# Kernel tuning notes

Measured on AMD Instinct MI355X. Metric: run time of the kernel, lower is better.

## Reference

```python
import jax, jax.numpy as jnp
import numpy as np

B, S, HID = 2, 4096, 640
NH, NKV, HD = 4, 1, 256
SCALING = 256.0 ** -0.5
SOFTCAP = 50.0
WINDOW = 512
EPS = 1e-6
ROPE_THETA = 10000.0  # local (sliding) rope base in Gemma3


def _rope_tables(seq_len, dim, theta):
    inv_freq = 1.0 / (theta ** (np.arange(0, dim, 2, dtype=np.float32) / dim))  # [dim/2]
    t = np.arange(seq_len, dtype=np.float32)
    freqs = np.outer(t, inv_freq)                      # [S, dim/2]
    emb = np.concatenate([freqs, freqs], axis=-1)      # [S, dim]
    return np.cos(emb)[None], np.sin(emb)[None]        # [1, S, dim]


def _sliding_causal_mask(b, s, window):
    i = np.arange(s)[:, None]
    j = np.arange(s)[None, :]
    allowed = (j <= i) & (j > i - window)              # causal + sliding window
    mask = np.where(allowed, 0.0, -1e9).astype(np.float32)
    return np.broadcast_to(mask[None, None], (b, 1, s, s)).copy()


def setup_inputs() -> dict:
    key = jax.random.key(0)
    ks = jax.random.split(key, 8)
    cos_np, sin_np = _rope_tables(S, HD, ROPE_THETA)
    return {
        "hidden_states": jax.random.normal(ks[0], (B, S, HID), jnp.float32),
        "cos": jnp.asarray(cos_np),
        "sin": jnp.asarray(sin_np),
        "attention_mask": jnp.asarray(_sliding_causal_mask(B, S, WINDOW)),
        "Wq": jax.random.normal(ks[1], (HID, NH * HD), jnp.float32) * 0.02,
        "Wk": jax.random.normal(ks[2], (HID, NKV * HD), jnp.float32) * 0.02,
        "Wv": jax.random.normal(ks[3], (HID, NKV * HD), jnp.float32) * 0.02,
        "Wo": jax.random.normal(ks[4], (NH * HD, HID), jnp.float32) * 0.02,
        "q_norm_w": jax.random.normal(ks[5], (HD,), jnp.float32) * 0.02,
        "k_norm_w": jax.random.normal(ks[6], (HD,), jnp.float32) * 0.02,
    }


def _rms_norm(x, w):
    var = jnp.mean(jnp.square(x), axis=-1, keepdims=True)
    return x * jax.lax.rsqrt(var + EPS) * (1.0 + w)


def _rotate_half(x):
    x1, x2 = jnp.split(x, 2, axis=-1)
    return jnp.concatenate([-x2, x1], axis=-1)


def _apply_rope(x, cos, sin):
    # x: [B, H, S, D]; cos/sin: [1, S, D] -> unsqueeze head dim
    c = cos[:, None, :, :]
    s = sin[:, None, :, :]
    return x * c + _rotate_half(x) * s


def reference(hidden_states, cos, sin, attention_mask, Wq, Wk, Wv, Wo, q_norm_w, k_norm_w):
    b, s, _ = hidden_states.shape
    # projections (no bias)
    q = (hidden_states @ Wq).reshape(b, s, NH, HD).transpose(0, 2, 1, 3)   # [B,NH,S,D]
    k = (hidden_states @ Wk).reshape(b, s, NKV, HD).transpose(0, 2, 1, 3)  # [B,1,S,D]
    v = (hidden_states @ Wv).reshape(b, s, NKV, HD).transpose(0, 2, 1, 3)  # [B,1,S,D]
    # per-head RMSNorm on q/k
    q = _rms_norm(q, q_norm_w)
    k = _rms_norm(k, k_norm_w)
    # RoPE
    q = _apply_rope(q, cos, sin)
    k = _apply_rope(k, cos, sin)
    # GQA: single kv head broadcast to all query heads
    k2 = k[:, 0]  # [B,S,D]
    v2 = v[:, 0]  # [B,S,D]
    scores = jnp.einsum('bhqd,bkd->bhqk', q, k2) * SCALING
    scores = SOFTCAP * jnp.tanh(scores / SOFTCAP)          # logit softcapping
    scores = scores + attention_mask                        # causal + sliding window
    attn = jax.nn.softmax(scores, axis=-1)
    out = jnp.einsum('bhqk,bkd->bhqd', attn, v2)            # [B,NH,S,D]
    out = out.transpose(0, 2, 1, 3).reshape(b, s, NH * HD)  # [B,S,NH*D]
    return out @ Wo                                         # [B,S,HID]
```

## Files before the change

### kernel.cpp

```cpp
#include <hip/hip_runtime.h>

typedef unsigned short u16;
typedef unsigned int u32;

typedef __attribute__((ext_vector_type(8)))  short bf16x8;
typedef __attribute__((ext_vector_type(4)))  float f32x4;

__device__ __forceinline__ float b2f(u16 u) {
    union { unsigned int i; float f; } v; v.i = ((unsigned int)u) << 16; return v.f;
}
__device__ __forceinline__ u16 f2b(float f) {
    union { float ff; unsigned int i; } v; v.ff = f;
    unsigned int x = v.i;
    return (u16)((x + 0x7fffu + ((x >> 16) & 1u)) >> 16);
}
__device__ __forceinline__ bool detect_bf16(const void* cosT) {
    return ((*(const u32*)cosT) & 0xffffu) == 0x3f80u;
}
__device__ __forceinline__ float4 ld4(const void* p, size_t off, bool isbf) {
    if (isbf) {
        ushort4 v = *(const ushort4*)((const u16*)p + off);
        return make_float4(b2f(v.x), b2f(v.y), b2f(v.z), b2f(v.w));
    }
    return *(const float4*)((const float*)p + off);
}
__device__ __forceinline__ float lds1(const void* p, size_t off, bool isbf) {
    return isbf ? b2f(((const u16*)p)[off]) : ((const float*)p)[off];
}
__device__ __forceinline__ void gll16(const void* g, void* l) {
    __builtin_amdgcn_global_load_lds(
        (const __attribute__((address_space(1))) u32*)g,
        (__attribute__((address_space(3))) u32*)l, 16, 0, 0);
}
__device__ __forceinline__ float capmask(float sdot, int i, int j) {
    float v = sdot * (0.0625f / 50.0f);
    v = fminf(fmaxf(v, -10.0f), 10.0f);
    float e = __expf(2.0f * v);
    float c = 50.0f * (e - 1.0f) / (e + 1.0f);
    bool allowed = (j <= i) && (j > i - 512);
    return allowed ? c : -1e30f;
}

__global__ __launch_bounds__(256) void prep(
    const void* __restrict__ hidden,
    const void* __restrict__ Wq, const void* __restrict__ Wk,
    const void* __restrict__ Wv, const void* __restrict__ Wo,
    const void* __restrict__ cosT,
    u16* __restrict__ Hb, u16* __restrict__ WT, u16* __restrict__ WoT)
{
    const bool isbf = detect_bf16(cosT);
    __shared__ float T[32][33];
    int id = blockIdx.x;
    if (id < 2560) {
        size_t base = ((size_t)id * 256 + threadIdx.x) * 8;
        if (isbf) {
            *(uint4*)(Hb + base) = *(const uint4*)((const u16*)hidden + base);
        } else {
            float4 a = ld4(hidden, base, false);
            float4 b = ld4(hidden, base + 4, false);
            uint4 o;
            o.x = (u32)f2b(a.x) | ((u32)f2b(a.y) << 16);
            o.y = (u32)f2b(a.z) | ((u32)f2b(a.w) << 16);
            o.z = (u32)f2b(b.x) | ((u32)f2b(b.y) << 16);
            o.w = (u32)f2b(b.z) | ((u32)f2b(b.w) << 16);
            *(uint4*)(Hb + base) = o;
        }
        return;
    }
    id -= 2560;
    const int tx = threadIdx.x & 31, ty = threadIdx.x >> 5;
    if (id < 960) {
        const int n0 = (id % 48) * 32, k0 = (id / 48) * 32;
        const void* src; int ldw, nof;
        if (n0 < 1024)      { src = Wq; ldw = 1024; nof = n0; }
        else if (n0 < 1280) { src = Wk; ldw = 256;  nof = n0 - 1024; }
        else                { src = Wv; ldw = 256;  nof = n0 - 1280; }
#pragma unroll
        for (int j = 0; j < 4; j++)
            T[ty + 8 * j][tx] = lds1(src, (size_t)(k0 + ty + 8 * j) * ldw + nof + tx, isbf);
        __syncthreads();
#pragma unroll
        for (int j = 0; j < 4; j++)
            WT[(size_t)(n0 + ty + 8 * j) * 640 + k0 + tx] = f2b(T[tx][ty + 8 * j]);
    } else {
        id -= 960;
        const int k0 = (id & 31) * 32, n0 = (id >> 5) * 32;
#pragma unroll
        for (int j = 0; j < 4; j++)
            T[ty + 8 * j][tx] = lds1(Wo, (size_t)(k0 + ty + 8 * j) * 640 + n0 + tx, isbf);
        __syncthreads();
#pragma unroll
        for (int j = 0; j < 4; j++)
            WoT[(size_t)(n0 + ty + 8 * j) * 1024 + k0 + tx] = f2b(T[tx][ty + 8 * j]);
    }
}

__global__ __launch_bounds__(256) void qkv_gemm(
    const u16* __restrict__ Hb, const u16* __restrict__ WT,
    u16* __restrict__ Qb, u16* __restrict__ Kb, u16* __restrict__ Vtg)
{
    const int n0 = blockIdx.x * 128, m0 = blockIdx.y * 128;
    const int t = threadIdx.x, w = t >> 6, lane = t & 63;
    const int l15 = lane & 15, quad = lane >> 4;
    const int wm = (w & 1) * 64, wn = (w >> 1) * 64;

    __shared__ __align__(16) char smem[33792];

    f32x4 acc[4][4];
#pragma unroll
    for (int i = 0; i < 4; i++)
#pragma unroll
        for (int j = 0; j < 4; j++) acc[i][j] = (f32x4)0.0f;

#pragma unroll
    for (int i = 0; i < 2; i++) {
        int ci = t + 256 * i, m = ci >> 2, c = ci & 3;
        gll16(Hb + (size_t)(m0 + m) * 640 + c * 8, smem + ci * 16);
        gll16(WT + (size_t)(n0 + m) * 640 + c * 8, smem + 8192 + ci * 16);
    }
    __syncthreads();

    for (int it = 0; it < 20; ++it) {
        const int kb = it * 32;
        char* cur = smem + (it & 1) * 16384;
        if (it < 19) {
            char* nxt = smem + ((it + 1) & 1) * 16384;
#pragma unroll
            for (int i = 0; i < 2; i++) {
                int ci = t + 256 * i, m = ci >> 2, c = ci & 3;
                gll16(Hb + (size_t)(m0 + m) * 640 + kb + 32 + c * 8, nxt + ci * 16);
                gll16(WT + (size_t)(n0 + m) * 640 + kb + 32 + c * 8, nxt + 8192 + ci * 16);
            }
        }
        const u16 (*Ah)[32] = (const u16 (*)[32])cur;
        const u16 (*Bh)[32] = (const u16 (*)[32])(cur + 8192);
        bf16x8 af[4], bfr[4];
#pragma unroll
        for (int mi = 0; mi < 4; mi++)
            af[mi] = *(const bf16x8*)&Ah[wm + mi * 16 + l15][quad * 8];
#pragma unroll
        for (int ni = 0; ni < 4; ni++)
            bfr[ni] = *(const bf16x8*)&Bh[wn + ni * 16 + l15][quad * 8];
#pragma unroll
        for (int mi = 0; mi < 4; mi++)
#pragma unroll
            for (int ni = 0; ni < 4; ni++)
                acc[mi][ni] = __builtin_amdgcn_mfma_f32_16x16x32_bf16(
                    af[mi], bfr[ni], acc[mi][ni], 0, 0, 0);
        __syncthreads();
    }

    if (n0 >= 1280) {
        const int bb = m0 >> 12, sblk = m0 & 4095;
#pragma unroll
        for (int mi = 0; mi < 4; mi++)
#pragma unroll
            for (int ni = 0; ni < 4; ni++) {
                int vd = n0 + wn + ni * 16 + l15 - 1280;
                int sb = sblk + wm + mi * 16 + quad * 4;
                ushort4 vv = make_ushort4(f2b(acc[mi][ni][0]), f2b(acc[mi][ni][1]),
                                          f2b(acc[mi][ni][2]), f2b(acc[mi][ni][3]));
                *(ushort4*)(Vtg + (size_t)bb * 1048576 + (size_t)vd * 4096 + sb) = vv;
            }
        return;
    }

    u16 (*Sc)[132] = (u16 (*)[132])smem;
#pragma unroll
    for (int mi = 0; mi < 4; mi++)
#pragma unroll
        for (int ni = 0; ni < 4; ni++)
#pragma unroll
            for (int r = 0; r < 4; r++)
                Sc[wm + mi * 16 + quad * 4 + r][wn + ni * 16 + l15] = f2b(acc[mi][ni][r]);
    __syncthreads();

    u16* dst; int ldo, coff;
    if (n0 < 1024) { dst = Qb; ldo = 1024; coff = n0; }
    else           { dst = Kb; ldo = 256;  coff = n0 - 1024; }
#pragma unroll
    for (int i = 0; i < 8; i++) {
        int idx = t + 256 * i, r = idx >> 4, c = idx & 15;
        *(uint4*)(dst + (size_t)(m0 + r) * ldo + coff + c * 8) = *(const uint4*)&Sc[r][c * 8];
    }
}

__global__ __launch_bounds__(320) void norm_rope(
    u16* __restrict__ Qb, u16* __restrict__ Kb,
    const void* __restrict__ cosT, const void* __restrict__ sinT,
    const void* __restrict__ qw, const void* __restrict__ kw)
{
    const bool isbf = detect_bf16(cosT);
    const int row = blockIdx.x, s = row & 4095;
    const int g = threadIdx.x >> 6, lane = threadIdx.x & 63, d0 = lane * 4;

    u16* p; const void* w;
    if (g < 4) { p = Qb + (size_t)row * 1024 + g * 256 + d0; w = qw; }
    else       { p = Kb + (size_t)row * 256 + d0;            w = kw; }

    ushort4 xv = *(const ushort4*)p;
    float x0 = b2f(xv.x), x1 = b2f(xv.y), x2 = b2f(xv.z), x3 = b2f(xv.w);
    float ssum = x0 * x0 + x1 * x1 + x2 * x2 + x3 * x3;
#pragma unroll
    for (int off = 32; off > 0; off >>= 1) ssum += __shfl_xor(ssum, off, 64);
    float rs = rsqrtf(ssum * (1.0f / 256.0f) + 1e-6f);

    float4 wv = ld4(w, d0, isbf);
    float n0 = x0 * rs * (1.0f + wv.x);
    float n1 = x1 * rs * (1.0f + wv.y);
    float n2 = x2 * rs * (1.0f + wv.z);
    float n3 = x3 * rs * (1.0f + wv.w);

    float o0 = __shfl_xor(n0, 32, 64);
    float o1 = __shfl_xor(n1, 32, 64);
    float o2 = __shfl_xor(n2, 32, 64);
    float o3 = __shfl_xor(n3, 32, 64);
    float sgn = (lane < 32) ? -1.0f : 1.0f;

    float4 cv = ld4(cosT, (size_t)s * 256 + d0, isbf);
    float4 sv = ld4(sinT, (size_t)s * 256 + d0, isbf);
    *(ushort4*)p = make_ushort4(
        f2b(n0 * cv.x + sgn * o0 * sv.x), f2b(n1 * cv.y + sgn * o1 * sv.y),
        f2b(n2 * cv.z + sgn * o2 * sv.z), f2b(n3 * cv.w + sgn * o3 * sv.w));
}

__global__ __launch_bounds__(512, 2) void attn_mfma(
    const u16* __restrict__ Qb, const u16* __restrict__ Kb,
    const u16* __restrict__ Vtg, u16* __restrict__ AO)
{
    const int bx = blockIdx.x;
    const int q0 = (((bx & 7) << 4) + (bx >> 3)) * 32;
    const int b  = blockIdx.y;
    const int t = threadIdx.x, w = t >> 6, lane = t & 63;
    const int h = w & 3, qh = w >> 2;
    const int l15 = lane & 15, quad = lane >> 4;
    const int qbase = q0 + qh * 16;
    const int swz = (l15 & 7) << 4;

    __shared__ __align__(16) u16 Ks[64][256];
    __shared__ __align__(16) u16 Vt[256][64];
    __shared__ __align__(16) u16 Pr[8][16][72];
    __shared__ float l_s[8][16];

    bf16x8 qf[8];
    {
        const u16* qp = Qb + ((size_t)(b * 4096 + qbase + l15)) * 1024 + h * 256 + quad * 8;
#pragma unroll
        for (int s = 0; s < 8; s++) qf[s] = *(const bf16x8*)(qp + s * 32);
    }

    f32x4 o[16];
#pragma unroll
    for (int i = 0; i < 16; i++) o[i] = (f32x4)0.0f;
    float lp[4] = {0.f, 0.f, 0.f, 0.f};

    const int lo = q0 - 511;
    const int jb0 = lo > 0 ? (lo >> 6) << 6 : 0;
    const int jb1 = (q0 + 31) & ~63;

    const u16* kbase = Kb + (size_t)b * 4096 * 256;
    const u16* vbase = Vtg + (size_t)b * 1048576;
    char* const ksb = (char*)&Ks[0][0];
    char* const vtb = (char*)&Vt[0][0];

    for (int jb = jb0; jb <= jb1; jb += 64) {
        __syncthreads();
#pragma unroll
        for (int i = 0; i < 4; i++) {
            int ci = t + 512 * i;
            int kr = ci >> 5, kc = ci & 31;
            *(uint4*)(ksb + kr * 512 + ((kc * 16) ^ ((kr & 7) << 4))) =
                *(const uint4*)(kbase + (size_t)(jb + kr) * 256 + kc * 8);
            int vr = ci >> 3, vc = ci & 7;
            *(uint4*)(vtb + vr * 128 + ((vc * 16) ^ ((vr & 7) << 4))) =
                *(const uint4*)(vbase + (size_t)vr * 4096 + jb + vc * 8);
        }
        __syncthreads();

        f32x4 s[4];
#pragma unroll
        for (int a = 0; a < 4; a++) s[a] = (f32x4)0.0f;
#pragma unroll
        for (int ds = 0; ds < 8; ds++) {
#pragma unroll
            for (int a = 0; a < 4; a++) {
                bf16x8 kf = *(const bf16x8*)(ksb + (a * 16 + l15) * 512 +
                                             (((ds * 4 + quad) * 16) ^ swz));
                s[a] = __builtin_amdgcn_mfma_f32_16x16x32_bf16(qf[ds], kf, s[a], 0, 0, 0);
            }
        }
#pragma unroll
        for (int ap = 0; ap < 2; ap++) {
            const int j0 = jb + ap * 32 + l15;
#pragma unroll
            for (int r = 0; r < 4; r++) {
                int qi = qbase + quad * 4 + r;
                float p0 = __expf(capmask(s[2 * ap][r],     qi, j0));
                float p1 = __expf(capmask(s[2 * ap + 1][r], qi, j0 + 16));
                u16 pb0 = f2b(p0), pb1 = f2b(p1);
                Pr[w][quad * 4 + r][ap * 32 + l15]      = pb0;
                Pr[w][quad * 4 + r][ap * 32 + 16 + l15] = pb1;
                lp[r] += b2f(pb0) + b2f(pb1);
            }
        }
        __threadfence_block();
        bf16x8 pf0 = *(const bf16x8*)&Pr[w][l15][quad * 8];
        bf16x8 pf1 = *(const bf16x8*)&Pr[w][l15][32 + quad * 8];
#pragma unroll
        for (int mt = 0; mt < 16; mt++) {
            bf16x8 vf0 = *(const bf16x8*)(vtb + (mt * 16 + l15) * 128 +
                                          ((quad * 16) ^ swz));
            o[mt] = __builtin_amdgcn_mfma_f32_16x16x32_bf16(vf0, pf0, o[mt], 0, 0, 0);
        }
#pragma unroll
        for (int mt = 0; mt < 16; mt++) {
            bf16x8 vf1 = *(const bf16x8*)(vtb + (mt * 16 + l15) * 128 +
                                          (((4 + quad) * 16) ^ swz));
            o[mt] = __builtin_amdgcn_mfma_f32_16x16x32_bf16(vf1, pf1, o[mt], 0, 0, 0);
        }
    }

#pragma unroll
    for (int r = 0; r < 4; r++) {
        float v = lp[r];
        v += __shfl_xor(v, 1, 64); v += __shfl_xor(v, 2, 64);
        v += __shfl_xor(v, 4, 64); v += __shfl_xor(v, 8, 64);
        lp[r] = v;
    }
    if (l15 == 0) {
#pragma unroll
        for (int r = 0; r < 4; r++) l_s[w][quad * 4 + r] = lp[r];
    }
    __threadfence_block();
    __syncthreads();
    const float inv = 1.0f / l_s[w][l15];

    u16* aop = AO + ((size_t)(b * 4096 + qbase + l15)) * 1024 + h * 256 + quad * 4;
#pragma unroll
    for (int mt = 0; mt < 16; mt++) {
        *(ushort4*)(aop + mt * 16) = make_ushort4(
            f2b(o[mt][0] * inv), f2b(o[mt][1] * inv),
            f2b(o[mt][2] * inv), f2b(o[mt][3] * inv));
    }
}

__global__ __launch_bounds__(256) void out_gemm(
    const u16* __restrict__ AO, const u16* __restrict__ WoT,
    const void* __restrict__ cosT, void* __restrict__ outp)
{
    const bool isbf = detect_bf16(cosT);
    const int n0 = blockIdx.x * 64, m0 = blockIdx.y * 128;
    const int t = threadIdx.x, w = t >> 6, lane = t & 63;
    const int l15 = lane & 15, quad = lane >> 4;
    const int wm = (w & 1) * 64, wn = (w >> 1) * 32;

    __shared__ __align__(16) char smem[34816];

    f32x4 acc[4][2];
#pragma unroll
    for (int i = 0; i < 4; i++)
#pragma unroll
        for (int j = 0; j < 2; j++) acc[i][j] = (f32x4)0.0f;

    {
#pragma unroll
        for (int i = 0; i < 2; i++) {
            int ci = t + 256 * i, m = ci >> 2, c = ci & 3;
            gll16(AO + (size_t)(m0 + m) * 1024 + c * 8, smem + ci * 16);
        }
        int m = t >> 2, c = t & 3;
        gll16(WoT + (size_t)(n0 + m) * 1024 + c * 8, smem + 8192 + t * 16);
    }
    __syncthreads();

    for (int it = 0; it < 32; ++it) {
        const int kb = it * 32;
        char* cur = smem + (it & 1) * 12288;
        if (it < 31) {
            char* nxt = smem + ((it + 1) & 1) * 12288;
#pragma unroll
            for (int i = 0; i < 2; i++) {
                int ci = t + 256 * i, m = ci >> 2, c = ci & 3;
                gll16(AO + (size_t)(m0 + m) * 1024 + kb + 32 + c * 8, nxt + ci * 16);
            }
            int m = t >> 2, c = t & 3;
            gll16(WoT + (size_t)(n0 + m) * 1024 + kb + 32 + c * 8, nxt + 8192 + t * 16);
        }
        const u16 (*Ah)[32] = (const u16 (*)[32])cur;
        const u16 (*Bh)[32] = (const u16 (*)[32])(cur + 8192);
        bf16x8 af[4], bfr[2];
#pragma unroll
        for (int mi = 0; mi < 4; mi++)
            af[mi] = *(const bf16x8*)&Ah[wm + mi * 16 + l15][quad * 8];
#pragma unroll
        for (int ni = 0; ni < 2; ni++)
            bfr[ni] = *(const bf16x8*)&Bh[wn + ni * 16 + l15][quad * 8];
#pragma unroll
        for (int mi = 0; mi < 4; mi++)
#pragma unroll
            for (int ni = 0; ni < 2; ni++)
                acc[mi][ni] = __builtin_amdgcn_mfma_f32_16x16x32_bf16(
                    af[mi], bfr[ni], acc[mi][ni], 0, 0, 0);
        __syncthreads();
    }

    float (*Scf)[68] = (float (*)[68])smem;
#pragma unroll
    for (int mi = 0; mi < 4; mi++)
#pragma unroll
        for (int ni = 0; ni < 2; ni++)
#pragma unroll
            for (int r = 0; r < 4; r++)
                Scf[wm + mi * 16 + quad * 4 + r][wn + ni * 16 + l15] = acc[mi][ni][r];
    __syncthreads();

    if (isbf) {
#pragma unroll
        for (int i = 0; i < 4; i++) {
            int idx = t + 256 * i, r = idx >> 3, c = idx & 7;
            ushort4 lo4 = make_ushort4(
                f2b(Scf[r][c * 8 + 0]), f2b(Scf[r][c * 8 + 1]),
                f2b(Scf[r][c * 8 + 2]), f2b(Scf[r][c * 8 + 3]));
            ushort4 hi4 = make_ushort4(
                f2b(Scf[r][c * 8 + 4]), f2b(Scf[r][c * 8 + 5]),
                f2b(Scf[r][c * 8 + 6]), f2b(Scf[r][c * 8 + 7]));
            u16* p = (u16*)outp + (size_t)(m0 + r) * 640 + n0 + c * 8;
            *(ushort4*)p = lo4; *(ushort4*)(p + 4) = hi4;
        }
    } else {
#pragma unroll
        for (int i = 0; i < 8; i++) {
            int idx = t + 256 * i, r = idx >> 4, c = idx & 15;
            float4 v = *(const float4*)&Scf[r][c * 4];
            *(float4*)((float*)outp + (size_t)(m0 + r) * 640 + n0 + c * 4) = v;
        }
    }
}

extern "C" void kernel_launch(void* const* d_in, const int* in_sizes, int n_in,
                              void* d_out, int out_size, void* d_ws, size_t ws_size,
                              hipStream_t stream) {
    const void* hidden = d_in[0];
    const void* cosT   = d_in[1];
    const void* sinT   = d_in[2];
    const void* Wq     = d_in[4];
    const void* Wk     = d_in[5];
    const void* Wv     = d_in[6];
    const void* Wo     = d_in[7];
    const void* qw     = d_in[8];
    const void* kw     = d_in[9];

    char* ws = (char*)d_ws;
    u16* Hb  = (u16*)ws;
    u16* WT  = (u16*)(ws + 10485760);
    u16* AO  = (u16*)ws;
    u16* WoT = (u16*)(ws + 16777216);
    u16* Qb  = (u16*)(ws + 18087936);
    u16* Kb  = (u16*)(ws + 34865152);
    u16* Vtg = (u16*)(ws + 39059456);

    prep<<<dim3(4160), 256, 0, stream>>>(hidden, Wq, Wk, Wv, Wo, cosT, Hb, WT, WoT);
    qkv_gemm<<<dim3(12, 64), 256, 0, stream>>>(Hb, WT, Qb, Kb, Vtg);
    norm_rope<<<dim3(8192), 320, 0, stream>>>(Qb, Kb, cosT, sinT, qw, kw);
    attn_mfma<<<dim3(128, 2), 512, 0, stream>>>(Qb, Kb, Vtg, AO);
    out_gemm<<<dim3(10, 64), 256, 0, stream>>>(AO, WoT, cosT, d_out);
}
```

Measured before the change: 310.3 us.

## Double-buffer K/V tiles with direct global-to-LDS loads in attention loop

Doubles the K and V shared-memory tiles and prefetches the next 64-key tile with direct global-to-LDS loads while the current tile is consumed by the MFMA score and PV loops. The XOR swizzle moves from the LDS destination to the global source address, so each thread writes a contiguous 16-byte chunk. Register-staged copies and the two __syncthreads per tile are replaced with explicit vmcnt/lgkmcnt waits and raw s_barrier. This is meant to hide global load latency and free registers, at the cost of roughly doubling the K/V LDS footprint, which may limit how many blocks fit per CU.

After: 310.9 us, median of 3. No clear change (+0.2%).

```diff
diff --git a/kernel.cpp b/kernel.cpp
--- a/kernel.cpp
+++ b/kernel.cpp
@@ -237,8 +237,8 @@
     const int qbase = q0 + qh * 16;
     const int swz = (l15 & 7) << 4;
 
-    __shared__ __align__(16) u16 Ks[64][256];
-    __shared__ __align__(16) u16 Vt[256][64];
+    __shared__ __align__(16) u16 KsD[2][64][256];
+    __shared__ __align__(16) u16 VtD[2][256][64];
     __shared__ __align__(16) u16 Pr[8][16][72];
     __shared__ float l_s[8][16];
 
@@ -257,25 +257,42 @@
     const int lo = q0 - 511;
     const int jb0 = lo > 0 ? (lo >> 6) << 6 : 0;
     const int jb1 = (q0 + 31) & ~63;
+    const int nt  = ((jb1 - jb0) >> 6) + 1;
 
     const u16* kbase = Kb + (size_t)b * 4096 * 256;
     const u16* vbase = Vtg + (size_t)b * 1048576;
-    char* const ksb = (char*)&Ks[0][0];
-    char* const vtb = (char*)&Vt[0][0];
-
-    for (int jb = jb0; jb <= jb1; jb += 64) {
-        __syncthreads();
-#pragma unroll
-        for (int i = 0; i < 4; i++) {
-            int ci = t + 512 * i;
-            int kr = ci >> 5, kc = ci & 31;
-            *(uint4*)(ksb + kr * 512 + ((kc * 16) ^ ((kr & 7) << 4))) =
-                *(const uint4*)(kbase + (size_t)(jb + kr) * 256 + kc * 8);
-            int vr = ci >> 3, vc = ci & 7;
-            *(uint4*)(vtb + vr * 128 + ((vc * 16) ^ ((vr & 7) << 4))) =
-                *(const uint4*)(vbase + (size_t)vr * 4096 + jb + vc * 8);
-        }
-        __syncthreads();
+
+#define STAGE_KV(jb_, bi_)                                                          \
+    {                                                                               \
+        char* kd = (char*)&KsD[bi_][0][0];                                          \
+        char* vd = (char*)&VtD[bi_][0][0];                                          \
+        _Pragma("unroll")                                                           \
+        for (int i_ = 0; i_ < 4; i_++) {                                            \
+            int ci = t + 512 * i_;                                                  \
+            int kr = ci >> 5, kc = ci & 31;                                         \
+            gll16(kbase + (size_t)((jb_) + kr) * 256 + ((kc ^ (kr & 7)) * 8),       \
+                  kd + ci * 16);                                                    \
+            int vr = ci >> 3, vc = ci & 7;                                          \
+            gll16(vbase + (size_t)vr * 4096 + (jb_) + ((vc ^ (vr & 7)) * 8),        \
+                  vd + ci * 16);                                                    \
+        }                                                                           \
+    }
+
+    STAGE_KV(jb0, 0);
+
+    for (int it = 0; it < nt; ++it) {
+        const int jb = jb0 + it * 64;
+        if (it + 1 < nt) {
+            STAGE_KV(jb + 64, (it + 1) & 1);
+            asm volatile("s_waitcnt vmcnt(8)" ::: "memory");
+        } else {
+            asm volatile("s_waitcnt vmcnt(0)" ::: "memory");
+        }
+        __builtin_amdgcn_s_barrier();
+        __builtin_amdgcn_sched_barrier(0);
+
+        const char* ksb = (const char*)&KsD[it & 1][0][0];
+        const char* vtb = (const char*)&VtD[it & 1][0][0];
 
         f32x4 s[4];
 #pragma unroll
@@ -318,7 +335,12 @@
                                           (((4 + quad) * 16) ^ swz));
             o[mt] = __builtin_amdgcn_mfma_f32_16x16x32_bf16(vf1, pf1, o[mt], 0, 0, 0);
         }
-    }
+
+        asm volatile("s_waitcnt lgkmcnt(0)" ::: "memory");
+        __builtin_amdgcn_s_barrier();
+        __builtin_amdgcn_sched_barrier(0);
+    }
+#undef STAGE_KV
 
 #pragma unroll
     for (int r = 0; r < 4; r++) {
```
